# Optimization experiments

Hardware: AMD Instinct MI355X
Metric: run time of the kernel (lower is better)

The kernel has to match this reference:

```python
import jax, jax.numpy as jnp
import numpy as np

B, L, D, I = 64, 196, 2048, 512

def setup_inputs() -> dict:
    key = jax.random.key(0)
    ks = jax.random.split(key, 8)
    s_f = 1.0 / np.sqrt(D)
    s_h = 1.0 / np.sqrt(I)
    s_a = 1.0 / np.sqrt(I)
    return {
        "feature_vectors": jax.random.normal(ks[0], (B, L, D), dtype=jnp.float32),
        "hidden_state": jax.random.normal(ks[1], (B, I), dtype=jnp.float32),
        "W_f": jax.random.uniform(ks[2], (D, I), jnp.float32, -s_f, s_f),
        "b_f": jax.random.uniform(ks[3], (I,), jnp.float32, -s_f, s_f),
        "W_h": jax.random.uniform(ks[4], (I, I), jnp.float32, -s_h, s_h),
        "b_h": jax.random.uniform(ks[5], (I,), jnp.float32, -s_h, s_h),
        "W_a": jax.random.uniform(ks[6], (I, D), jnp.float32, -s_a, s_a),
        "b_a": jax.random.uniform(ks[7], (D,), jnp.float32, -s_a, s_a),
    }

def reference(feature_vectors, hidden_state, W_f, b_f, W_h, b_h, W_a, b_a):
    # fv: [B,L,D], hidden: [B,I]
    fv_shaped = jnp.einsum('bld,di->bli', feature_vectors, W_f) + b_f      # [B,L,I]
    hs_shaped = hidden_state @ W_h + b_h                                   # [B,I]
    e = jnp.einsum('bli,id->bld', fv_shaped + hs_shaped[:, None, :], W_a) + b_a  # [B,L,D]
    alpha = jax.nn.softmax(e, axis=1)                                      # softmax over L locations
    z = jnp.sum(alpha * feature_vectors, axis=1)                           # [B,D] (vectorized loop)
    return (z, alpha)
```

## Files before the change

kernel.cpp:

```cpp
#include <hip/hip_runtime.h>

#define B_ 64
#define L_ 196
#define D_ 2048
#define I_ 512
#define M_ (B_*L_)

typedef __attribute__((ext_vector_type(8))) short bf16x8;
typedef __attribute__((ext_vector_type(4))) float f32x4;
typedef unsigned short u16;

__device__ __forceinline__ u16 f2bf(float x){
  unsigned u = __float_as_uint(x);
  u += 0x7fffu + ((u >> 16) & 1u);
  return (u16)(u >> 16);
}

__device__ __forceinline__ void gld16(const void* g, void* l){
  __builtin_amdgcn_global_load_lds(
      (const __attribute__((address_space(1))) void*)g,
      (__attribute__((address_space(3))) void*)l, 16, 0, 0);
}

template<int N> __device__ __forceinline__ void wait_vm(){
  __builtin_amdgcn_s_waitcnt((N&15) | ((N&48)<<10) | (7<<4) | (15<<8));
}
__device__ __forceinline__ void wait_lgkm0(){
  __builtin_amdgcn_s_waitcnt(15 | (48<<10) | (7<<4));
}
__device__ __forceinline__ void bar(){
  asm volatile("" ::: "memory");
  __builtin_amdgcn_s_barrier();
  asm volatile("" ::: "memory");
}

__global__ void cvt_bf16_kernel(const float* __restrict__ in, u16* __restrict__ out, int n4){
  int i = blockIdx.x*blockDim.x + threadIdx.x;
  int stride = gridDim.x*blockDim.x;
  for (; i < n4; i += stride){
    float4 v = ((const float4*)in)[i];
    ushort4 o;
    o.x = f2bf(v.x); o.y = f2bf(v.y); o.z = f2bf(v.z); o.w = f2bf(v.w);
    ((ushort4*)out)[i] = o;
  }
}

__global__ void transpose_cvt_kernel(const float* __restrict__ in, u16* __restrict__ out, int R, int C){
  __shared__ float tile[32][33];
  int c0 = blockIdx.x*32, r0 = blockIdx.y*32;
  int tx = threadIdx.x, ty = threadIdx.y;
  for (int i=0;i<32;i+=8)
    tile[ty+i][tx] = in[(size_t)(r0+ty+i)*C + c0 + tx];
  __syncthreads();
  for (int i=0;i<32;i+=8)
    out[(size_t)(c0+ty+i)*R + r0 + tx] = f2bf(tile[tx][ty+i]);
}

__launch_bounds__(256)
__global__ void hs_kernel(const float* __restrict__ hidden, const float* __restrict__ Wh,
                          const float* __restrict__ bh, float* __restrict__ hs){
  __shared__ float red[4][64];
  const int nl = threadIdx.x & 63, kg = threadIdx.x >> 6;
  const int n = blockIdx.x*64 + nl, b = blockIdx.y;
  const float* hrow = hidden + b*I_;
  float a0=0.f, a1=0.f;
  #pragma unroll
  for (int k=kg*128; k<kg*128+128; k+=2){
    a0 = fmaf(hrow[k+0], Wh[(size_t)(k+0)*I_ + n], a0);
    a1 = fmaf(hrow[k+1], Wh[(size_t)(k+1)*I_ + n], a1);
  }
  red[kg][nl] = a0 + a1;
  __syncthreads();
  if (kg == 0)
    hs[b*I_ + n] = bh[n] + (red[0][nl]+red[1][nl]) + (red[2][nl]+red[3][nl]);
}

__launch_bounds__(256)
__global__ void gemm1_kernel(const u16* __restrict__ A, const u16* __restrict__ Bt,
                             const float* __restrict__ bias, const float* __restrict__ hs,
                             u16* __restrict__ outb)
{
  constexpr int K = D_, BK = 64, NIT = K/BK;
  __shared__ __align__(16) u16 Als[2][64*64];
  __shared__ __align__(16) u16 Bls[2][128*64];

  const int tid = threadIdx.x, lane = tid&63, wave = tid>>6;
  const int m0 = blockIdx.y*64, n0 = blockIdx.x*128;
  const int q = lane>>4, mr = lane&15;
  const int wrow = (wave&1)*32, wcol = (wave>>1)*64;
  const int lrow = lane>>3, kc = (lane&7)^lrow;

  const u16* Ag[2]; int Alo[2];
  #pragma unroll
  for (int u=0;u<2;++u){ int j = wave*2+u; Ag[u] = A + (size_t)(m0 + j*8 + lrow)*K + kc*8; Alo[u] = j*512; }
  const u16* Bg[4]; int Blo[4];
  #pragma unroll
  for (int u=0;u<4;++u){ int j = wave*4+u; Bg[u] = Bt + (size_t)(n0 + j*8 + lrow)*K + kc*8; Blo[u] = j*512; }

  int aoff[2][2], boff[4][2];
  #pragma unroll
  for (int i=0;i<2;i++)
    #pragma unroll
    for (int s=0;s<2;s++){ int R = wrow + i*16 + mr; aoff[i][s] = R*64 + (((s*4+q) ^ (mr&7))*8); }
  #pragma unroll
  for (int j=0;j<4;j++)
    #pragma unroll
    for (int s=0;s<2;s++){ int C = wcol + j*16 + mr; boff[j][s] = C*64 + (((s*4+q) ^ (mr&7))*8); }

  f32x4 acc[2][4];
  #pragma unroll
  for (int i=0;i<2;i++)
    #pragma unroll
    for (int j=0;j<4;j++) acc[i][j] = (f32x4){0.f,0.f,0.f,0.f};

  #pragma unroll
  for (int u=0;u<2;++u) gld16(Ag[u],    &Als[0][Alo[u]]);
  #pragma unroll
  for (int u=0;u<4;++u) gld16(Bg[u],    &Bls[0][Blo[u]]);
  #pragma unroll
  for (int u=0;u<2;++u) gld16(Ag[u]+BK, &Als[1][Alo[u]]);
  #pragma unroll
  for (int u=0;u<4;++u) gld16(Bg[u]+BK, &Bls[1][Blo[u]]);

  for (int i=0;i<NIT;++i){
    if (i+1<NIT) wait_vm<6>(); else wait_vm<0>();
    bar();
    const u16* Ab = Als[i&1];
    const u16* Bb = Bls[i&1];
    bf16x8 af[2][2], bg[4][2];
    #pragma unroll
    for (int s=0;s<2;s++){
      #pragma unroll
      for (int i2=0;i2<2;i2++) af[i2][s] = *(const bf16x8*)(Ab + aoff[i2][s]);
      #pragma unroll
      for (int j=0;j<4;j++)    bg[j][s]  = *(const bf16x8*)(Bb + boff[j][s]);
    }
    wait_lgkm0();
    bar();
    if (i+2<NIT){
      int k0 = (i+2)*BK;
      #pragma unroll
      for (int u=0;u<2;++u) gld16(Ag[u]+k0, &Als[i&1][Alo[u]]);
      #pragma unroll
      for (int u=0;u<4;++u) gld16(Bg[u]+k0, &Bls[i&1][Blo[u]]);
    }
    #pragma unroll
    for (int s=0;s<2;s++)
      #pragma unroll
      for (int i2=0;i2<2;i2++)
        #pragma unroll
        for (int j=0;j<4;j++)
          acc[i2][j] = __builtin_amdgcn_mfma_f32_16x16x32_bf16(af[i2][s], bg[j][s], acc[i2][j], 0,0,0);
  }

  #pragma unroll
  for (int i2=0;i2<2;i2++){
    #pragma unroll
    for (int j=0;j<4;j++){
      int gcol = n0 + wcol + j*16 + mr;
      float bcol = bias[gcol];
      #pragma unroll
      for (int r=0;r<4;r++){
        int grow = m0 + wrow + i2*16 + q*4 + r;
        int batch = grow / L_;
        outb[(size_t)grow*I_ + gcol] = f2bf(acc[i2][j][r] + bcol + hs[batch*I_ + gcol]);
      }
    }
  }
}

__launch_bounds__(256)
__global__ void gemm2_fused_kernel(const u16* __restrict__ T, const u16* __restrict__ Wa,
                                   const float* __restrict__ b_a, const float* __restrict__ fv,
                                   float* __restrict__ out)
{
  constexpr int K = I_, BK = 32, NIT = K/BK;
  __shared__ __align__(16) u16 Als[2][256*32];
  __shared__ __align__(16) u16 Bls[2][64*32];

  const int tid = threadIdx.x, lane = tid&63, wave = tid>>6;
  const int b = blockIdx.y, n0 = blockIdx.x*64;
  const int q = lane>>4, mr = lane&15;
  const int l16 = lane>>2, kc4 = (lane&3)^(l16&3);

  const u16* Ag[4]; int Alo[4];
  #pragma unroll
  for (int u=0;u<4;++u){
    int j = wave*4+u;
    int grow = b*L_ + j*16 + l16; if (grow > M_-1) grow = M_-1;
    Ag[u] = T + (size_t)grow*K + kc4*8; Alo[u] = j*512;
  }
  const u16* Bg = Wa + (size_t)(n0 + wave*16 + l16)*K + kc4*8;
  const int  Blo = wave*512;

  const int abase = mr*32 + ((q ^ (mr&3))*8);
  const int col  = n0 + wave*16 + mr;
  const int boff = col - n0 == (wave*16+mr) ? ((wave*16+mr)*32 + ((q ^ (mr&3))*8)) : 0;

  f32x4 acc[13];
  #pragma unroll
  for (int i=0;i<13;i++) acc[i] = (f32x4){0,0,0,0};

  #pragma unroll
  for (int u=0;u<4;++u) gld16(Ag[u],    &Als[0][Alo[u]]);
  gld16(Bg,    &Bls[0][Blo]);
  #pragma unroll
  for (int u=0;u<4;++u) gld16(Ag[u]+BK, &Als[1][Alo[u]]);
  gld16(Bg+BK, &Bls[1][Blo]);

  for (int it=0; it<NIT; ++it){
    if (it+1<NIT) wait_vm<5>(); else wait_vm<0>();
    bar();
    const u16* Ab = Als[it&1];
    const u16* Bb = Bls[it&1];
    bf16x8 bg0 = *(const bf16x8*)(Bb + boff);
    bf16x8 af[13];
    #pragma unroll
    for (int i=0;i<13;++i) af[i] = *(const bf16x8*)(Ab + abase + i*512);
    wait_lgkm0();
    bar();
    if (it+2<NIT){
      int k0 = (it+2)*BK;
      #pragma unroll
      for (int u=0;u<4;++u) gld16(Ag[u]+k0, &Als[it&1][Alo[u]]);
      gld16(Bg+k0, &Bls[it&1][Blo]);
    }
    #pragma unroll
    for (int i=0;i<13;++i)
      acc[i] = __builtin_amdgcn_mfma_f32_16x16x32_bf16(af[i], bg0, acc[i], 0,0,0);
  }

  const bool v12 = (q == 0);
  float bc = b_a[col];
  #pragma unroll
  for (int i=0;i<13;++i)
    #pragma unroll
    for (int r=0;r<4;++r) acc[i][r] += bc;

  float m = -3.4e38f;
  #pragma unroll
  for (int i=0;i<12;++i)
    #pragma unroll
    for (int r=0;r<4;++r) m = fmaxf(m, acc[i][r]);
  if (v12)
    #pragma unroll
    for (int r=0;r<4;++r) m = fmaxf(m, acc[12][r]);
  m = fmaxf(m, __shfl_xor(m, 16));
  m = fmaxf(m, __shfl_xor(m, 32));

  float s = 0.f;
  #pragma unroll
  for (int i=0;i<12;++i)
    #pragma unroll
    for (int r=0;r<4;++r){ float e = __expf(acc[i][r]-m); acc[i][r] = e; s += e; }
  if (v12)
    #pragma unroll
    for (int r=0;r<4;++r){ float e = __expf(acc[12][r]-m); acc[12][r] = e; s += e; }
  s += __shfl_xor(s, 16);
  s += __shfl_xor(s, 32);
  float inv = 1.f/s;

  float* alpha = out + (size_t)B_*D_ + (size_t)b*L_*D_;
  const float* fvb = fv + (size_t)b*L_*D_;
  float z = 0.f;
  #pragma unroll
  for (int i=0;i<13;++i){
    if (i < 12 || v12){
      #pragma unroll
      for (int r=0;r<4;++r){
        int row = i*16 + q*4 + r;
        float a = acc[i][r] * inv;
        alpha[(size_t)row*D_ + col] = a;
        z = fmaf(a, fvb[(size_t)row*D_ + col], z);
      }
    }
  }
  z += __shfl_xor(z, 16);
  z += __shfl_xor(z, 32);
  if (q == 0) out[(size_t)b*D_ + col] = z;
}

extern "C" void kernel_launch(void* const* d_in, const int* in_sizes, int n_in,
                              void* d_out, int out_size, void* d_ws, size_t ws_size,
                              hipStream_t stream){
  (void)in_sizes; (void)n_in; (void)out_size; (void)ws_size;
  const float* fv     = (const float*)d_in[0];
  const float* hidden = (const float*)d_in[1];
  const float* W_f    = (const float*)d_in[2];
  const float* b_f    = (const float*)d_in[3];
  const float* W_h    = (const float*)d_in[4];
  const float* b_h    = (const float*)d_in[5];
  const float* W_a    = (const float*)d_in[6];
  const float* b_a    = (const float*)d_in[7];
  float* out = (float*)d_out;

  char* ws = (char*)d_ws;
  u16*   fv_bf = (u16*)ws;
  u16*   t_bf  = (u16*)(ws + 51380224);
  u16*   WfT   = (u16*)(ws + 64225280);
  u16*   WaT   = (u16*)(ws + 66322432);
  float* hsbuf = (float*)(ws + 68419584);

  cvt_bf16_kernel<<<4096, 256, 0, stream>>>(fv, fv_bf, (B_*L_*D_)/4);
  transpose_cvt_kernel<<<dim3(I_/32, D_/32), dim3(32,8), 0, stream>>>(W_f, WfT, D_, I_);
  transpose_cvt_kernel<<<dim3(D_/32, I_/32), dim3(32,8), 0, stream>>>(W_a, WaT, I_, D_);
  hs_kernel<<<dim3(I_/64, B_), 256, 0, stream>>>(hidden, W_h, b_h, hsbuf);

  gemm1_kernel<<<dim3(I_/128, M_/64), 256, 0, stream>>>(fv_bf, WfT, b_f, hsbuf, t_bf);
  gemm2_fused_kernel<<<dim3(D_/64, B_), 256, 0, stream>>>(t_bf, WaT, b_a, fv, out);
}
```

Before: 332.4 us.

## Prefetch feature vectors during GEMM loop and interleave LDS reads with MFMAs

```diff
diff --git a/kernel.cpp b/kernel.cpp
--- a/kernel.cpp
+++ b/kernel.cpp
@@ -28,10 +28,16 @@
 __device__ __forceinline__ void wait_lgkm0(){
   __builtin_amdgcn_s_waitcnt(15 | (48<<10) | (7<<4));
 }
+template<int N> __device__ __forceinline__ void wait_lgkm(){
+  __builtin_amdgcn_s_waitcnt(15 | (48<<10) | (7<<4) | ((N&15)<<8));
+}
 __device__ __forceinline__ void bar(){
   asm volatile("" ::: "memory");
   __builtin_amdgcn_s_barrier();
   asm volatile("" ::: "memory");
+}
+__device__ __forceinline__ void fence_sched(){
+  __builtin_amdgcn_sched_barrier(0);
 }
 
 __global__ void cvt_bf16_kernel(const float* __restrict__ in, u16* __restrict__ out, int n4){
@@ -169,7 +175,7 @@
   }
 }
 
-__launch_bounds__(256)
+__launch_bounds__(256, 2)
 __global__ void gemm2_fused_kernel(const u16* __restrict__ T, const u16* __restrict__ Wa,
                                    const float* __restrict__ b_a, const float* __restrict__ fv,
                                    float* __restrict__ out)
@@ -181,7 +187,8 @@
   const int tid = threadIdx.x, lane = tid&63, wave = tid>>6;
   const int b = blockIdx.y, n0 = blockIdx.x*64;
   const int q = lane>>4, mr = lane&15;
-  const int l16 = lane>>2, kc4 = (lane&3)^(l16&3);
+  const int l16 = lane>>2;
+  const int kc4 = ((lane&3) ^ (l16&3) ^ (l16>>2)) & 3;
 
   const u16* Ag[4]; int Alo[4];
   #pragma unroll
@@ -193,9 +200,13 @@
   const u16* Bg = Wa + (size_t)(n0 + wave*16 + l16)*K + kc4*8;
   const int  Blo = wave*512;
 
-  const int abase = mr*32 + ((q ^ (mr&3))*8);
-  const int col  = n0 + wave*16 + mr;
-  const int boff = col - n0 == (wave*16+mr) ? ((wave*16+mr)*32 + ((q ^ (mr&3))*8)) : 0;
+  const int rsw   = ((mr&3) ^ (mr>>2)) & 3;
+  const int abase = mr*32 + (((q ^ rsw)&3)*8);
+  const int col   = n0 + wave*16 + mr;
+  const int boff  = (wave*16+mr)*32 + (((q ^ rsw)&3)*8);
+
+  const float* fvB = fv + (size_t)b*L_*D_;
+  float fvr[52];
 
   f32x4 acc[13];
   #pragma unroll
@@ -208,16 +219,35 @@
   for (int u=0;u<4;++u) gld16(Ag[u]+BK, &Als[1][Alo[u]]);
   gld16(Bg+BK, &Bls[1][Blo]);
 
+  #pragma unroll
   for (int it=0; it<NIT; ++it){
-    if (it+1<NIT) wait_vm<5>(); else wait_vm<0>();
+    if      (it == 0)     wait_vm<5>();
+    else if (it == 1)     wait_vm<9>();
+    else if (it == NIT-1) wait_vm<0>();
+    else if (it == NIT-2) wait_vm<9>();
+    else                  wait_vm<13>();
     bar();
     const u16* Ab = Als[it&1];
     const u16* Bb = Bls[it&1];
     bf16x8 bg0 = *(const bf16x8*)(Bb + boff);
     bf16x8 af[13];
     #pragma unroll
-    for (int i=0;i<13;++i) af[i] = *(const bf16x8*)(Ab + abase + i*512);
-    wait_lgkm0();
+    for (int i=0;i<8;++i) af[i] = *(const bf16x8*)(Ab + abase + i*512);
+    wait_lgkm<4>(); fence_sched();
+    #pragma unroll
+    for (int i=0;i<4;++i) acc[i] = __builtin_amdgcn_mfma_f32_16x16x32_bf16(af[i], bg0, acc[i], 0,0,0);
+    fence_sched();
+    #pragma unroll
+    for (int i=8;i<12;++i) af[i] = *(const bf16x8*)(Ab + abase + i*512);
+    wait_lgkm<4>(); fence_sched();
+    #pragma unroll
+    for (int i=4;i<8;++i) acc[i] = __builtin_amdgcn_mfma_f32_16x16x32_bf16(af[i], bg0, acc[i], 0,0,0);
+    fence_sched();
+    af[12] = *(const bf16x8*)(Ab + abase + 12*512);
+    wait_lgkm<1>(); fence_sched();
+    #pragma unroll
+    for (int i=8;i<12;++i) acc[i] = __builtin_amdgcn_mfma_f32_16x16x32_bf16(af[i], bg0, acc[i], 0,0,0);
+    wait_lgkm<0>(); fence_sched();
     bar();
     if (it+2<NIT){
       int k0 = (it+2)*BK;
@@ -225,10 +255,22 @@
       for (int u=0;u<4;++u) gld16(Ag[u]+k0, &Als[it&1][Alo[u]]);
       gld16(Bg+k0, &Bls[it&1][Blo]);
     }
-    #pragma unroll
-    for (int i=0;i<13;++i)
-      acc[i] = __builtin_amdgcn_mfma_f32_16x16x32_bf16(af[i], bg0, acc[i], 0,0,0);
-  }
+    fence_sched();
+    if (it < 12){
+      #pragma unroll
+      for (int r=0;r<4;++r)
+        fvr[it*4+r] = __builtin_nontemporal_load(&fvB[(size_t)(it*16 + q*4 + r)*D_ + col]);
+    } else if (it == 12){
+      #pragma unroll
+      for (int r=0;r<4;++r){
+        int row = 192 + q*4 + r; if (row > L_-1) row = L_-1;
+        fvr[48+r] = __builtin_nontemporal_load(&fvB[(size_t)row*D_ + col]);
+      }
+    }
+    fence_sched();
+    acc[12] = __builtin_amdgcn_mfma_f32_16x16x32_bf16(af[12], bg0, acc[12], 0,0,0);
+  }
+  fence_sched();
 
   const bool v12 = (q == 0);
   float bc = b_a[col];
@@ -261,18 +303,24 @@
   float inv = 1.f/s;
 
   float* alpha = out + (size_t)B_*D_ + (size_t)b*L_*D_;
-  const float* fvb = fv + (size_t)b*L_*D_;
   float z = 0.f;
   #pragma unroll
-  for (int i=0;i<13;++i){
-    if (i < 12 || v12){
-      #pragma unroll
-      for (int r=0;r<4;++r){
-        int row = i*16 + q*4 + r;
-        float a = acc[i][r] * inv;
-        alpha[(size_t)row*D_ + col] = a;
-        z = fmaf(a, fvb[(size_t)row*D_ + col], z);
-      }
+  for (int i=0;i<12;++i){
+    #pragma unroll
+    for (int r=0;r<4;++r){
+      int row = i*16 + q*4 + r;
+      float a = acc[i][r] * inv;
+      __builtin_nontemporal_store(a, &alpha[(size_t)row*D_ + col]);
+      z = fmaf(a, fvr[i*4+r], z);
+    }
+  }
+  if (v12){
+    #pragma unroll
+    for (int r=0;r<4;++r){
+      int row = 192 + r;
+      float a = acc[12][r] * inv;
+      __builtin_nontemporal_store(a, &alpha[(size_t)row*D_ + col]);
+      z = fmaf(a, fvr[48+r], z);
     }
   }
   z += __shfl_xor(z, 16);
```

Result: no change. 334.4 us (+0.6%).

## Fuse fp32-to-bf16 conversion of feature vectors into gemm1 operand load

Applied to the files above, without the earlier changes.

```diff
diff --git a/kernel.cpp b/kernel.cpp
--- a/kernel.cpp
+++ b/kernel.cpp
@@ -32,17 +32,6 @@
   asm volatile("" ::: "memory");
   __builtin_amdgcn_s_barrier();
   asm volatile("" ::: "memory");
-}
-
-__global__ void cvt_bf16_kernel(const float* __restrict__ in, u16* __restrict__ out, int n4){
-  int i = blockIdx.x*blockDim.x + threadIdx.x;
-  int stride = gridDim.x*blockDim.x;
-  for (; i < n4; i += stride){
-    float4 v = ((const float4*)in)[i];
-    ushort4 o;
-    o.x = f2bf(v.x); o.y = f2bf(v.y); o.z = f2bf(v.z); o.w = f2bf(v.w);
-    ((ushort4*)out)[i] = o;
-  }
 }
 
 __global__ void transpose_cvt_kernel(const float* __restrict__ in, u16* __restrict__ out, int R, int C){
@@ -76,81 +65,101 @@
 }
 
 __launch_bounds__(256)
-__global__ void gemm1_kernel(const u16* __restrict__ A, const u16* __restrict__ Bt,
+__global__ void gemm1_kernel(const float* __restrict__ A, const u16* __restrict__ Bt,
                              const float* __restrict__ bias, const float* __restrict__ hs,
                              u16* __restrict__ outb)
 {
-  constexpr int K = D_, BK = 64, NIT = K/BK;
-  __shared__ __align__(16) u16 Als[2][64*64];
-  __shared__ __align__(16) u16 Bls[2][128*64];
+  constexpr int K = D_, BK = 32, NIT = K/BK;
+  __shared__ __align__(16) float Als[2][64*32];
+  __shared__ __align__(16) u16  Bls[2][128*32];
 
   const int tid = threadIdx.x, lane = tid&63, wave = tid>>6;
   const int m0 = blockIdx.y*64, n0 = blockIdx.x*128;
   const int q = lane>>4, mr = lane&15;
   const int wrow = (wave&1)*32, wcol = (wave>>1)*64;
-  const int lrow = lane>>3, kc = (lane&7)^lrow;
-
-  const u16* Ag[2]; int Alo[2];
-  #pragma unroll
-  for (int u=0;u<2;++u){ int j = wave*2+u; Ag[u] = A + (size_t)(m0 + j*8 + lrow)*K + kc*8; Alo[u] = j*512; }
-  const u16* Bg[4]; int Blo[4];
-  #pragma unroll
-  for (int u=0;u<4;++u){ int j = wave*4+u; Bg[u] = Bt + (size_t)(n0 + j*8 + lrow)*K + kc*8; Blo[u] = j*512; }
-
-  int aoff[2][2], boff[4][2];
+
+  const int arow = lane>>3, achk = (lane&7)^arow;
+  const float* Ag[2]; int Alo[2];
+  #pragma unroll
+  for (int u=0;u<2;++u){
+    int j = wave*2+u;
+    Ag[u] = A + (size_t)(m0 + j*8 + arow)*K + achk*4;
+    Alo[u] = j*256;
+  }
+  const int brow = lane>>2, bchk = (lane&3)^(brow&3);
+  const u16* Bg[2]; int Blo[2];
+  #pragma unroll
+  for (int u=0;u<2;++u){
+    int j = wave*2+u;
+    Bg[u] = Bt + (size_t)(n0 + j*16 + brow)*K + bchk*8;
+    Blo[u] = j*512;
+  }
+
+  int afoff[2][2], bgoff[4];
+  #pragma unroll
+  for (int i2=0;i2<2;i2++)
+    #pragma unroll
+    for (int p=0;p<2;p++){
+      int R = wrow + i2*16 + mr;
+      afoff[i2][p] = R*32 + (((2*q+p) ^ (mr&7))*4);
+    }
+  #pragma unroll
+  for (int j=0;j<4;j++){
+    int C = wcol + j*16 + mr;
+    bgoff[j] = C*32 + ((q ^ (mr&3))*8);
+  }
+
+  f32x4 acc[2][4];
   #pragma unroll
   for (int i=0;i<2;i++)
     #pragma unroll
-    for (int s=0;s<2;s++){ int R = wrow + i*16 + mr; aoff[i][s] = R*64 + (((s*4+q) ^ (mr&7))*8); }
-  #pragma unroll
-  for (int j=0;j<4;j++)
-    #pragma unroll
-    for (int s=0;s<2;s++){ int C = wcol + j*16 + mr; boff[j][s] = C*64 + (((s*4+q) ^ (mr&7))*8); }
-
-  f32x4 acc[2][4];
-  #pragma unroll
-  for (int i=0;i<2;i++)
-    #pragma unroll
     for (int j=0;j<4;j++) acc[i][j] = (f32x4){0.f,0.f,0.f,0.f};
 
   #pragma unroll
   for (int u=0;u<2;++u) gld16(Ag[u],    &Als[0][Alo[u]]);
   #pragma unroll
-  for (int u=0;u<4;++u) gld16(Bg[u],    &Bls[0][Blo[u]]);
+  for (int u=0;u<2;++u) gld16(Bg[u],    &Bls[0][Blo[u]]);
   #pragma unroll
   for (int u=0;u<2;++u) gld16(Ag[u]+BK, &Als[1][Alo[u]]);
   #pragma unroll
-  for (int u=0;u<4;++u) gld16(Bg[u]+BK, &Bls[1][Blo[u]]);
-
-  for (int i=0;i<NIT;++i){
-    if (i+1<NIT) wait_vm<6>(); else wait_vm<0>();
+  for (int u=0;u<2;++u) gld16(Bg[u]+BK, &Bls[1][Blo[u]]);
+
+  for (int it=0; it<NIT; ++it){
+    if (it+1<NIT) wait_vm<4>(); else wait_vm<0>();
     bar();
-    const u16* Ab = Als[i&1];
-    const u16* Bb = Bls[i&1];
-    bf16x8 af[2][2], bg[4][2];
-    #pragma unroll
-    for (int s=0;s<2;s++){
-      #pragma unroll
-      for (int i2=0;i2<2;i2++) af[i2][s] = *(const bf16x8*)(Ab + aoff[i2][s]);
-      #pragma unroll
-      for (int j=0;j<4;j++)    bg[j][s]  = *(const bf16x8*)(Bb + boff[j][s]);
-    }
+    const float* Ab = Als[it&1];
+    const u16*   Bb = Bls[it&1];
+    f32x4 a0[2], a1[2]; bf16x8 bg[4];
+    #pragma unroll
+    for (int i2=0;i2<2;i2++){
+      a0[i2] = *(const f32x4*)(Ab + afoff[i2][0]);
+      a1[i2] = *(const f32x4*)(Ab + afoff[i2][1]);
+    }
+    #pragma unroll
+    for (int j=0;j<4;j++) bg[j] = *(const bf16x8*)(Bb + bgoff[j]);
     wait_lgkm0();
     bar();
-    if (i+2<NIT){
-      int k0 = (i+2)*BK;
-      #pragma unroll
-      for (int u=0;u<2;++u) gld16(Ag[u]+k0, &Als[i&1][Alo[u]]);
-      #pragma unroll
-      for (int u=0;u<4;++u) gld16(Bg[u]+k0, &Bls[i&1][Blo[u]]);
-    }
-    #pragma unroll
-    for (int s=0;s<2;s++)
-      #pragma unroll
-      for (int i2=0;i2<2;i2++)
-        #pragma unroll
-        for (int j=0;j<4;j++)
-          acc[i2][j] = __builtin_amdgcn_mfma_f32_16x16x32_bf16(af[i2][s], bg[j][s], acc[i2][j], 0,0,0);
+    if (it+2<NIT){
+      int k0 = (it+2)*BK;
+      #pragma unroll
+      for (int u=0;u<2;++u) gld16(Ag[u]+k0, &Als[it&1][Alo[u]]);
+      #pragma unroll
+      for (int u=0;u<2;++u) gld16(Bg[u]+k0, &Bls[it&1][Blo[u]]);
+    }
+    bf16x8 af[2];
+    #pragma unroll
+    for (int i2=0;i2<2;i2++){
+      #pragma unroll
+      for (int e=0;e<4;e++){
+        af[i2][e]   = (short)f2bf(a0[i2][e]);
+        af[i2][4+e] = (short)f2bf(a1[i2][e]);
+      }
+    }
+    #pragma unroll
+    for (int i2=0;i2<2;i2++)
+      #pragma unroll
+      for (int j=0;j<4;j++)
+        acc[i2][j] = __builtin_amdgcn_mfma_f32_16x16x32_bf16(af[i2], bg[j], acc[i2][j], 0,0,0);
   }
 
   #pragma unroll
@@ -195,7 +204,7 @@
 
   const int abase = mr*32 + ((q ^ (mr&3))*8);
   const int col  = n0 + wave*16 + mr;
-  const int boff = col - n0 == (wave*16+mr) ? ((wave*16+mr)*32 + ((q ^ (mr&3))*8)) : 0;
+  const int boff = (wave*16+mr)*32 + ((q ^ (mr&3))*8);
 
   f32x4 acc[13];
   #pragma unroll
@@ -295,17 +304,15 @@
   float* out = (float*)d_out;
 
   char* ws = (char*)d_ws;
-  u16*   fv_bf = (u16*)ws;
-  u16*   t_bf  = (u16*)(ws + 51380224);
-  u16*   WfT   = (u16*)(ws + 64225280);
-  u16*   WaT   = (u16*)(ws + 66322432);
-  float* hsbuf = (float*)(ws + 68419584);
-
-  cvt_bf16_kernel<<<4096, 256, 0, stream>>>(fv, fv_bf, (B_*L_*D_)/4);
+  u16*   t_bf  = (u16*)ws;
+  u16*   WfT   = (u16*)(ws + 12845056);
+  u16*   WaT   = (u16*)(ws + 14942208);
+  float* hsbuf = (float*)(ws + 17039360);
+
   transpose_cvt_kernel<<<dim3(I_/32, D_/32), dim3(32,8), 0, stream>>>(W_f, WfT, D_, I_);
   transpose_cvt_kernel<<<dim3(D_/32, I_/32), dim3(32,8), 0, stream>>>(W_a, WaT, I_, D_);
   hs_kernel<<<dim3(I_/64, B_), 256, 0, stream>>>(hidden, W_h, b_h, hsbuf);
 
-  gemm1_kernel<<<dim3(I_/128, M_/64), 256, 0, stream>>>(fv_bf, WfT, b_f, hsbuf, t_bf);
+  gemm1_kernel<<<dim3(I_/128, M_/64), 256, 0, stream>>>(fv, WfT, b_f, hsbuf, t_bf);
   gemm2_fused_kernel<<<dim3(D_/64, B_), 256, 0, stream>>>(t_bf, WaT, b_a, fv, out);
 }
```

Result: no change. 336.2 us (+1.1%).
